# Kernel optimization log

Measured on AMD Instinct MI355X. Metric: run time of the kernel, lower is better.

The kernel has to match this reference:

```python
import jax, jax.numpy as jnp
import numpy as np

N = 100000


def gcn_conv(x, W, b, src, dst, deg_inv_sqrt, n):
    # PyG GCNConv: h = D^{-1/2} (A + I) D^{-1/2} (x W) + b
    h = x @ W  # [N, out]
    norm = deg_inv_sqrt[src] * deg_inv_sqrt[dst]  # [E+N]
    msgs = h[src] * norm[:, None]  # gathered + scaled messages
    out = jax.ops.segment_sum(msgs, dst, num_segments=n)
    return out + b


def _self_loops_and_norm(edge_index, n):
    src, dst = edge_index[0], edge_index[1]
    loop = jnp.arange(n, dtype=edge_index.dtype)
    src = jnp.concatenate([src, loop])
    dst = jnp.concatenate([dst, loop])
    deg = jax.ops.segment_sum(jnp.ones_like(dst, dtype=jnp.float32), dst, num_segments=n)
    deg_inv_sqrt = jnp.where(deg > 0, jax.lax.rsqrt(jnp.maximum(deg, 1.0)), 0.0)
    return src, dst, deg_inv_sqrt


def setup_inputs() -> dict:
    key = jax.random.key(0)
    k1, k2, k3, k4 = jax.random.split(key, 4)
    nfeat, nhid, nclass = 512, 256, 40
    E = 3200000
    x = jax.random.normal(k1, (N, nfeat), dtype=jnp.float32)
    edge_index = jax.random.randint(k2, (2, E), 0, N, dtype=jnp.int64)
    # Glorot-style init for GCNConv weights, zero bias (PyG default)
    W1 = jax.random.normal(k3, (nfeat, nhid), dtype=jnp.float32) / np.sqrt(nfeat)
    b1 = jnp.zeros((nhid,), dtype=jnp.float32)
    W2 = jax.random.normal(k4, (nhid, nclass), dtype=jnp.float32) / np.sqrt(nhid)
    b2 = jnp.zeros((nclass,), dtype=jnp.float32)
    return {"x": x, "W1": W1, "b1": b1, "W2": W2, "b2": b2, "edge_index": edge_index}


def reference(x, W1, b1, W2, b2, edge_index):
    src, dst, dis = _self_loops_and_norm(edge_index, N)
    h = gcn_conv(x, W1, b1, src, dst, dis, N)
    h = jax.nn.relu(h)
    # dropout(p=0.5) is identity in eval mode
    h = gcn_conv(h, W2, b2, src, dst, dis, N)
    return jax.nn.log_softmax(h, axis=1)
```

## Files before the change

kernel.cpp:

```cpp
#include <hip/hip_runtime.h>
#include <math.h>

#define NFEAT 512
#define NHID  256
#define NCLASS 40
#define NBUCK 782
#define BCAP  5120
#define PCHUNK 8192

typedef __attribute__((ext_vector_type(8))) short short8;
typedef __attribute__((ext_vector_type(4))) float f32x4;


__device__ __forceinline__ float bflo(unsigned u) {
    union { unsigned i; float f; } x; x.i = u << 16; return x.f;
}
__device__ __forceinline__ float bfhi(unsigned u) {
    union { unsigned i; float f; } x; x.i = u & 0xffff0000u; return x.f;
}
__device__ __forceinline__ unsigned short f2bf(float f) {
    union { float f; unsigned i; } x; x.f = f;
    unsigned r = x.i + 0x7fffu + ((x.i >> 16) & 1u);
    return (unsigned short)(r >> 16);
}
__device__ __forceinline__ float bf2f(unsigned short h) {
    union { unsigned i; float f; } x; x.i = (unsigned)h << 16; return x.f;
}
__device__ __forceinline__ unsigned pack2(float a, float b) {
    return (unsigned)f2bf(a) | ((unsigned)f2bf(b) << 16);
}


__global__ __launch_bounds__(256) void partcast_k(const float* __restrict__ W1,
                                                  unsigned short* __restrict__ WT,
                                                  const float* __restrict__ W2,
                                                  unsigned short* __restrict__ WT2,
                                                  const int* __restrict__ ei,
                                                  int* bucketCnt,
                                                  unsigned* __restrict__ binned, int E) {
    __shared__ unsigned staged[PCHUNK];
    __shared__ int hist[NBUCK];
    __shared__ int lofs[NBUCK];
    __shared__ int sbase[NBUCK];
    __shared__ int lcur[NBUCK];
    __shared__ int wsum[256];
    int bid = blockIdx.x;
    int t = threadIdx.x;
    if (bid < (NFEAT * NHID) / 256) {
        int idx = bid * 256 + t;
        int k = idx >> 8;
        int nn = idx & 255;
        WT[(size_t)nn * NFEAT + k] = f2bf(W1[idx]);
        return;
    }
    if (bid == (NFEAT * NHID) / 256) {
        for (int idx = t; idx < 96 * 256; idx += 256) {
            int j2 = idx >> 8;
            int k = idx & 255;
            int j = (j2 < 48) ? j2 : j2 - 48;
            float v = (j < NCLASS) ? W2[k * NCLASS + j] : 0.f;
            unsigned short hi = f2bf(v);
            WT2[idx] = (j2 < 48) ? hi : f2bf(v - bf2f(hi));
        }
        return;
    }
    int pb = bid - (NFEAT * NHID) / 256 - 1;
    int beg = pb * PCHUNK;
    int end = beg + PCHUNK; if (end > E) end = E;

    for (int b = t; b < NBUCK; b += 256) hist[b] = 0;
    __syncthreads();
    for (int e = beg + t; e < end; e += 256) {
        int d = ei[(size_t)E + e];
        atomicAdd(&hist[d >> 7], 1);
    }
    __syncthreads();
    int v[4];
    int s0 = 0;
#pragma unroll
    for (int r = 0; r < 4; ++r) {
        int idx = t * 4 + r;
        v[r] = (idx < NBUCK) ? hist[idx] : 0;
        s0 += v[r];
    }
    wsum[t] = s0;
    __syncthreads();
    for (int off = 1; off < 256; off <<= 1) {
        int add = (t >= off) ? wsum[t - off] : 0;
        __syncthreads();
        wsum[t] += add;
        __syncthreads();
    }
    int excl = wsum[t] - s0;
#pragma unroll
    for (int r = 0; r < 4; ++r) {
        int idx = t * 4 + r;
        if (idx < NBUCK) { lofs[idx] = excl; lcur[idx] = excl; }
        excl += v[r];
    }
    __syncthreads();
    for (int b = t; b < NBUCK; b += 256) {
        int h = hist[b];
        if (h) sbase[b] = atomicAdd(&bucketCnt[b], h);
    }
    for (int e = beg + t; e < end; e += 256) {
        int s = ei[e];
        int d = ei[(size_t)E + e];
        int b = d >> 7;
        int p = atomicAdd(&lcur[b], 1);
        staged[p] = ((unsigned)s << 7) | (unsigned)(d & 127);
    }
    __syncthreads();
    int w = t >> 6, lane = t & 63;
    for (int b = w; b < NBUCK; b += 4) {
        int h = hist[b];
        if (!h) continue;
        int lo = lofs[b];
        size_t gb = (size_t)b * BCAP + sbase[b];
        for (int l = lane; l < h; l += 64)
            binned[gb + l] = staged[lo + l];
    }
}


__global__ __launch_bounds__(1024) void bscan_k(const int* __restrict__ bucketCnt,
                                                int* __restrict__ bbase,
                                                int* __restrict__ offs, int n, int E) {
    __shared__ int sd[1024];
    int t = threadIdx.x;
    int v = (t < NBUCK) ? bucketCnt[t] : 0;
    sd[t] = v;
    __syncthreads();
    for (int off = 1; off < 1024; off <<= 1) {
        int add = (t >= off) ? sd[t - off] : 0;
        __syncthreads();
        sd[t] += add;
        __syncthreads();
    }
    if (t < NBUCK) bbase[t] = sd[t] - v;
    if (t == 0) offs[n] = E;
}


__global__ __launch_bounds__(512) void fill2_k(const unsigned* __restrict__ binned,
                                               const int* __restrict__ bucketCnt,
                                               const int* __restrict__ bbase,
                                               int* __restrict__ offs,
                                               float* __restrict__ dis,
                                               int* __restrict__ csrs, int n) {
    __shared__ int h128[128];
    __shared__ int sd[128];
    __shared__ int lcur[128];
    int b = blockIdx.x;
    int t = threadIdx.x;
    int node0 = b << 7;
    int cbt = bucketCnt[b];
    size_t base_in = (size_t)b * BCAP;
    int gbase = bbase[b];
    if (t < 128) h128[t] = 0;
    __syncthreads();
    for (int e = t; e < cbt; e += 512) {
        unsigned u = binned[base_in + e];
        atomicAdd(&h128[u & 127], 1);
    }
    __syncthreads();
    int v = (t < 128) ? h128[t] : 0;
    if (t < 128) sd[t] = v;
    __syncthreads();
    for (int off = 1; off < 128; off <<= 1) {
        int add = (t < 128 && t >= off) ? sd[t - off] : 0;
        __syncthreads();
        if (t < 128) sd[t] += add;
        __syncthreads();
    }
    if (t < 128) {
        int excl = sd[t] - v;
        int nd = node0 + t;
        if (nd < n) {
            offs[nd] = gbase + excl;
            dis[nd] = rsqrtf((float)v + 1.0f);
        }
        lcur[t] = gbase + excl;
    }
    __syncthreads();
    for (int e = t; e < cbt; e += 512) {
        unsigned u = binned[base_in + e];
        int pos = atomicAdd(&lcur[u & 127], 1);
        csrs[pos] = (int)(u >> 7);
    }
}


__global__ __launch_bounds__(512) void gemm1_k(const float* __restrict__ X,
                                               const unsigned short* __restrict__ WT,
                                               const float* __restrict__ dis,
                                               unsigned short* __restrict__ H, int M) {
    __shared__ unsigned short as[128][72];
    __shared__ unsigned short bs[256][72];
    int t = threadIdx.x;
    int lane = t & 63;
    int w = t >> 6;
    int wm = w >> 2;
    int wn = w & 3;
    int m0 = blockIdx.x * 128;
    int quad = lane >> 4;
    int r16 = lane & 15;

    f32x4 acc[4][4];
#pragma unroll
    for (int a = 0; a < 4; ++a)
#pragma unroll
        for (int b = 0; b < 4; ++b) acc[a][b] = (f32x4){0.f, 0.f, 0.f, 0.f};

    for (int k0 = 0; k0 < NFEAT; k0 += 64) {
        {
            int m = t >> 2;
            int c = (t & 3) * 16;
            int gi = m0 + m;
            float4 v0, v1, v2, v3;
            if (gi < M) {
                const float4* p = (const float4*)(X + (size_t)gi * NFEAT + k0 + c);
                v0 = p[0]; v1 = p[1]; v2 = p[2]; v3 = p[3];
            } else {
                v0 = v1 = v2 = v3 = make_float4(0.f, 0.f, 0.f, 0.f);
            }
            uint4 p0, p1;
            p0.x = pack2(v0.x, v0.y); p0.y = pack2(v0.z, v0.w);
            p0.z = pack2(v1.x, v1.y); p0.w = pack2(v1.z, v1.w);
            p1.x = pack2(v2.x, v2.y); p1.y = pack2(v2.z, v2.w);
            p1.z = pack2(v3.x, v3.y); p1.w = pack2(v3.z, v3.w);
            *(uint4*)&as[m][c] = p0;
            *(uint4*)&as[m][c + 8] = p1;
        }
        {
            int row = t >> 1;
            int ch = (t & 1) * 32;
            const uint4* p = (const uint4*)(WT + (size_t)row * NFEAT + k0 + ch);
#pragma unroll
            for (int c = 0; c < 4; ++c) {
                uint4 q = p[c];
                *(uint4*)&bs[row][ch + c * 8] = q;
            }
        }
        __syncthreads();
#pragma unroll
        for (int ks = 0; ks < 64; ks += 32) {
            short8 af[4], bfr[4];
#pragma unroll
            for (int sm = 0; sm < 4; ++sm)
                af[sm] = *(const short8*)&as[wm * 64 + sm * 16 + r16][ks + quad * 8];
#pragma unroll
            for (int sn = 0; sn < 4; ++sn)
                bfr[sn] = *(const short8*)&bs[wn * 64 + sn * 16 + r16][ks + quad * 8];
#pragma unroll
            for (int sm = 0; sm < 4; ++sm)
#pragma unroll
                for (int sn = 0; sn < 4; ++sn)
                    acc[sm][sn] = __builtin_amdgcn_mfma_f32_16x16x32_bf16(
                        af[sm], bfr[sn], acc[sm][sn], 0, 0, 0);
        }
        __syncthreads();
    }
#pragma unroll
    for (int sm = 0; sm < 4; ++sm) {
#pragma unroll
        for (int rr = 0; rr < 4; ++rr) {
            int row = m0 + wm * 64 + sm * 16 + quad * 4 + rr;
            if (row < M) {
                float dsc = dis[row];
#pragma unroll
                for (int sn = 0; sn < 4; ++sn) {
                    int col = wn * 64 + sn * 16 + r16;
                    H[(size_t)row * NHID + col] = f2bf(acc[sm][sn][rr] * dsc);
                }
            }
        }
    }
}


__global__ __launch_bounds__(256) void agg1h_k(const unsigned short* __restrict__ Hb,
                                               const int* __restrict__ offs,
                                               const int* __restrict__ csrs,
                                               const float* __restrict__ dis,
                                               const float* __restrict__ b1,
                                               unsigned short* __restrict__ outb,
                                               int n, int f0u) {
    int lane = threadIdx.x & 63;
    int i = blockIdx.x * 4 + (threadIdx.x >> 6);
    if (i >= n) return;
    const unsigned* Hv = (const unsigned*)Hb;
    int col = f0u + lane;
    float a0 = 0.f, a1 = 0.f;
    int beg = offs[i], end = offs[i + 1];
    int e = beg;
    {
        int c[16]; unsigned g[16];
        for (; e + 16 <= end; e += 16) {
#pragma unroll
            for (int u = 0; u < 16; ++u) c[u] = csrs[e + u];
#pragma unroll
            for (int u = 0; u < 16; ++u) g[u] = Hv[(size_t)c[u] * 128 + col];
#pragma unroll
            for (int u = 0; u < 16; ++u) {
                a0 += bflo(g[u]); a1 += bfhi(g[u]);
            }
        }
        if (e < end) {
#pragma unroll
            for (int u = 0; u < 16; ++u)
                c[u] = (e + u < end) ? csrs[e + u] : i;
#pragma unroll
            for (int u = 0; u < 16; ++u) g[u] = Hv[(size_t)c[u] * 128 + col];
#pragma unroll
            for (int u = 0; u < 16; ++u) {
                float sel = (e + u < end) ? 1.f : 0.f;
                a0 = fmaf(sel, bflo(g[u]), a0); a1 = fmaf(sel, bfhi(g[u]), a1);
            }
        }
    }
    unsigned v = Hv[(size_t)i * 128 + col];
    a0 += bflo(v); a1 += bfhi(v);
    float di = dis[i];
    float2 bb = ((const float2*)b1)[col];
    a0 = fmaxf(fmaf(a0, di, bb.x), 0.f);
    a1 = fmaxf(fmaf(a1, di, bb.y), 0.f);
    ((unsigned*)outb)[(size_t)i * 128 + col] = pack2(a0, a1);
}


__global__ __launch_bounds__(256) void gemm2_k(const unsigned short* __restrict__ Ab,
                                               const unsigned short* __restrict__ WT2,
                                               const float* __restrict__ dis,
                                               unsigned short* __restrict__ H2b, int M) {
    __shared__ unsigned short wt2s[96][264];
    int t = threadIdx.x;
    int lane = t & 63;
    int w = t >> 6;
    int quad = lane >> 4;
    int r16 = lane & 15;
    for (int idx = t; idx < 96 * 32; idx += 256) {
        int r = idx >> 5;
        int c = idx & 31;
        *(uint4*)&wt2s[r][c * 8] = ((const uint4*)(WT2 + (size_t)r * 256))[c];
    }
    __syncthreads();
    int row0 = blockIdx.x * 64 + w * 16;
    int gr = row0 + r16;
    f32x4 acc[3];
#pragma unroll
    for (int sn = 0; sn < 3; ++sn) acc[sn] = (f32x4){0.f, 0.f, 0.f, 0.f};
#pragma unroll
    for (int ks = 0; ks < 8; ++ks) {
        short8 af;
        if (gr < M)
            af = *(const short8*)(Ab + (size_t)gr * NHID + ks * 32 + quad * 8);
        else
            af = (short8){0, 0, 0, 0, 0, 0, 0, 0};
#pragma unroll
        for (int sn = 0; sn < 3; ++sn) {
            short8 bhi = *(const short8*)&wt2s[sn * 16 + r16][ks * 32 + quad * 8];
            short8 blo = *(const short8*)&wt2s[48 + sn * 16 + r16][ks * 32 + quad * 8];
            acc[sn] = __builtin_amdgcn_mfma_f32_16x16x32_bf16(af, bhi, acc[sn], 0, 0, 0);
            acc[sn] = __builtin_amdgcn_mfma_f32_16x16x32_bf16(af, blo, acc[sn], 0, 0, 0);
        }
    }
#pragma unroll
    for (int rr = 0; rr < 4; ++rr) {
        int row = row0 + quad * 4 + rr;
        if (row < M) {
            float dsc = dis[row];
#pragma unroll
            for (int sn = 0; sn < 3; ++sn)
                H2b[(size_t)row * 64 + sn * 16 + r16] = f2bf(acc[sn][rr] * dsc);
        }
    }
    if (lane < 32) {
        int row = row0 + r16;
        if (row < M)
            *(uint4*)&H2b[(size_t)row * 64 + 48 + (lane >> 4) * 8] =
                make_uint4(0u, 0u, 0u, 0u);
    }
}


__global__ __launch_bounds__(256) void agg2_k(const unsigned short* __restrict__ H2b,
                                              const int* __restrict__ offs,
                                              const int* __restrict__ csrs,
                                              const float* __restrict__ dis,
                                              const float* __restrict__ b2,
                                              float* __restrict__ out, int n) {
    int lane = threadIdx.x & 63;
    int i = blockIdx.x * 4 + (threadIdx.x >> 6);
    if (i >= n) return;
    const uint2* Hv = (const uint2*)H2b;
    int slot = lane >> 4;
    int r16 = lane & 15;
    float a0 = 0.f, a1 = 0.f, a2 = 0.f, a3 = 0.f;
    int beg = offs[i], end = offs[i + 1];
    int e = beg;
    {
        int c[8]; uint2 g[8];
        for (; e + 32 <= end; e += 32) {
#pragma unroll
            for (int u = 0; u < 8; ++u) c[u] = csrs[e + u * 4 + slot];
#pragma unroll
            for (int u = 0; u < 8; ++u) g[u] = Hv[(size_t)c[u] * 16 + r16];
#pragma unroll
            for (int u = 0; u < 8; ++u) {
                a0 += bflo(g[u].x); a1 += bfhi(g[u].x);
                a2 += bflo(g[u].y); a3 += bfhi(g[u].y);
            }
        }
        if (e < end) {
#pragma unroll
            for (int u = 0; u < 8; ++u) {
                int idx = e + u * 4 + slot;
                c[u] = (idx < end) ? csrs[idx] : i;
            }
#pragma unroll
            for (int u = 0; u < 8; ++u) g[u] = Hv[(size_t)c[u] * 16 + r16];
#pragma unroll
            for (int u = 0; u < 8; ++u) {
                float sel = (e + u * 4 + slot < end) ? 1.f : 0.f;
                a0 = fmaf(sel, bflo(g[u].x), a0); a1 = fmaf(sel, bfhi(g[u].x), a1);
                a2 = fmaf(sel, bflo(g[u].y), a2); a3 = fmaf(sel, bfhi(g[u].y), a3);
            }
        }
    }
    if (slot == 0) {
        uint2 v = Hv[(size_t)i * 16 + r16];
        a0 += bflo(v.x); a1 += bfhi(v.x);
        a2 += bflo(v.y); a3 += bfhi(v.y);
    }
    a0 += __shfl_xor(a0, 16, 64); a0 += __shfl_xor(a0, 32, 64);
    a1 += __shfl_xor(a1, 16, 64); a1 += __shfl_xor(a1, 32, 64);
    a2 += __shfl_xor(a2, 16, 64); a2 += __shfl_xor(a2, 32, 64);
    a3 += __shfl_xor(a3, 16, 64); a3 += __shfl_xor(a3, 32, 64);
    float di = dis[i];
    bool act = (r16 < 10);
    float4 bb = act ? ((const float4*)b2)[r16] : make_float4(0.f, 0.f, 0.f, 0.f);
    a0 = fmaf(a0, di, bb.x); a1 = fmaf(a1, di, bb.y);
    a2 = fmaf(a2, di, bb.z); a3 = fmaf(a3, di, bb.w);
    float m = act ? fmaxf(fmaxf(a0, a1), fmaxf(a2, a3)) : -INFINITY;
#pragma unroll
    for (int off = 8; off > 0; off >>= 1) m = fmaxf(m, __shfl_xor(m, off, 16));
    float s = act ? (expf(a0 - m) + expf(a1 - m) + expf(a2 - m) + expf(a3 - m)) : 0.f;
#pragma unroll
    for (int off = 8; off > 0; off >>= 1) s += __shfl_xor(s, off, 16);
    float ls = m + logf(s);
    if (lane < 10) {
        float4 o = make_float4(a0 - ls, a1 - ls, a2 - ls, a3 - ls);
        ((float4*)(out + (size_t)i * NCLASS))[lane] = o;
    }
}


extern "C" void kernel_launch(void* const* d_in, const int* in_sizes, int n_in,
                              void* d_out, int out_size, void* d_ws, size_t ws_size,
                              hipStream_t stream) {
    const float* x  = (const float*)d_in[0];
    const float* W1 = (const float*)d_in[1];
    const float* b1 = (const float*)d_in[2];
    const float* W2 = (const float*)d_in[3];
    const float* b2 = (const float*)d_in[4];
    const int*   ei = (const int*)d_in[5];

    const int N = in_sizes[0] / NFEAT;
    const int E = in_sizes[5] / 2;

    size_t off = 0;
    auto alloc = [&](size_t bytes) { size_t o = off; off += (bytes + 255) & ~(size_t)255; return o; };
    char* ws = (char*)d_ws;
    int*            offs    = (int*)           (ws + alloc((size_t)(N + 1) * 4));
    float*          dis     = (float*)         (ws + alloc((size_t)N * 4));
    int*            bcnt    = (int*)           (ws + alloc((size_t)NBUCK * 4));
    int*            bbase   = (int*)           (ws + alloc((size_t)NBUCK * 4));
    unsigned*       binned  = (unsigned*)      (ws + alloc((size_t)NBUCK * BCAP * 4));
    int*            csrs    = (int*)           (ws + alloc((size_t)E * 4));
    unsigned short* wT      = (unsigned short*)(ws + alloc((size_t)NFEAT * NHID * 2));
    unsigned short* wT2     = (unsigned short*)(ws + alloc((size_t)96 * 256 * 2));
    unsigned short* h1b     = (unsigned short*)(ws + alloc((size_t)N * NHID * 2));
    unsigned short* a1b     = (unsigned short*)(ws + alloc((size_t)N * NHID * 2));
    unsigned short* h2b     = (unsigned short*)(ws + alloc((size_t)N * 64 * 2));
    float*          out     = (float*)d_out;

    int npart = (E + PCHUNK - 1) / PCHUNK;

    hipMemsetAsync(bcnt, 0, (size_t)NBUCK * 4, stream);
    partcast_k<<<(NFEAT * NHID) / 256 + 1 + npart, 256, 0, stream>>>(W1, wT, W2, wT2, ei,
                                                                     bcnt, binned, E);
    bscan_k<<<1, 1024, 0, stream>>>(bcnt, bbase, offs, N, E);
    fill2_k<<<NBUCK, 512, 0, stream>>>(binned, bcnt, bbase, offs, dis, csrs, N);
    gemm1_k<<<(N + 127) / 128, 512, 0, stream>>>(x, wT, dis, h1b, N);
    agg1h_k<<<(N + 3) / 4, 256, 0, stream>>>(h1b, offs, csrs, dis, b1, a1b, N, 0);
    agg1h_k<<<(N + 3) / 4, 256, 0, stream>>>(h1b, offs, csrs, dis, b1, a1b, N, 64);
    gemm2_k<<<(N + 63) / 64, 256, 0, stream>>>(a1b, wT2, dis, h2b, N);
    agg2_k<<<(N + 3) / 4, 256, 0, stream>>>(h2b, offs, csrs, dis, b2, out, N);
}
```

Baseline: 715.8 us.

## Load GEMM1 operands directly from global into MFMA fragments, dropping LDS staging

The first-layer GEMM no longer stages X and W tiles through shared memory with block-wide barriers. Each wave reads its A rows (fp32, converted to bf16 in registers) and B rows straight from global memory into MFMA fragments, looping over K in 32-wide steps. This removes the LDS traffic and syncthreads, but each X row is now fetched by four waves and the per-lane loads are strided row reads, so L2/global traffic rises and coalescing worsens.

```diff
diff --git a/kernel.cpp b/kernel.cpp
--- a/kernel.cpp
+++ b/kernel.cpp
@@ -195,14 +195,12 @@
                                                const unsigned short* __restrict__ WT,
                                                const float* __restrict__ dis,
                                                unsigned short* __restrict__ H, int M) {
-    __shared__ unsigned short as[128][72];
-    __shared__ unsigned short bs[256][72];
     int t = threadIdx.x;
     int lane = t & 63;
     int w = t >> 6;
     int wm = w >> 2;
     int wn = w & 3;
-    int m0 = blockIdx.x * 128;
+    int m0 = blockIdx.x * 128 + wm * 64;
     int quad = lane >> 4;
     int r16 = lane & 15;
 
@@ -212,60 +210,49 @@
 #pragma unroll
         for (int b = 0; b < 4; ++b) acc[a][b] = (f32x4){0.f, 0.f, 0.f, 0.f};
 
-    for (int k0 = 0; k0 < NFEAT; k0 += 64) {
-        {
-            int m = t >> 2;
-            int c = (t & 3) * 16;
-            int gi = m0 + m;
-            float4 v0, v1, v2, v3;
-            if (gi < M) {
-                const float4* p = (const float4*)(X + (size_t)gi * NFEAT + k0 + c);
-                v0 = p[0]; v1 = p[1]; v2 = p[2]; v3 = p[3];
+    const unsigned short* wbase = WT + (size_t)(wn * 64 + r16) * NFEAT + quad * 8;
+    const float* abase[4];
+    bool okA[4];
+#pragma unroll
+    for (int sm = 0; sm < 4; ++sm) {
+        int row = m0 + sm * 16 + r16;
+        okA[sm] = (row < M);
+        abase[sm] = X + (size_t)(okA[sm] ? row : 0) * NFEAT + quad * 8;
+    }
+
+#pragma unroll 2
+    for (int ks = 0; ks < 16; ++ks) {
+        int ko = ks * 32;
+        short8 bfr[4];
+#pragma unroll
+        for (int sn = 0; sn < 4; ++sn)
+            bfr[sn] = *(const short8*)(wbase + (size_t)sn * 16 * NFEAT + ko);
+#pragma unroll
+        for (int sm = 0; sm < 4; ++sm) {
+            short8 af;
+            if (okA[sm]) {
+                const float4* p = (const float4*)(abase[sm] + ko);
+                float4 v0 = p[0], v1 = p[1];
+                union { uint4 u; short8 s; } cv;
+                cv.u.x = pack2(v0.x, v0.y);
+                cv.u.y = pack2(v0.z, v0.w);
+                cv.u.z = pack2(v1.x, v1.y);
+                cv.u.w = pack2(v1.z, v1.w);
+                af = cv.s;
             } else {
-                v0 = v1 = v2 = v3 = make_float4(0.f, 0.f, 0.f, 0.f);
-            }
-            uint4 p0, p1;
-            p0.x = pack2(v0.x, v0.y); p0.y = pack2(v0.z, v0.w);
-            p0.z = pack2(v1.x, v1.y); p0.w = pack2(v1.z, v1.w);
-            p1.x = pack2(v2.x, v2.y); p1.y = pack2(v2.z, v2.w);
-            p1.z = pack2(v3.x, v3.y); p1.w = pack2(v3.z, v3.w);
-            *(uint4*)&as[m][c] = p0;
-            *(uint4*)&as[m][c + 8] = p1;
-        }
-        {
-            int row = t >> 1;
-            int ch = (t & 1) * 32;
-            const uint4* p = (const uint4*)(WT + (size_t)row * NFEAT + k0 + ch);
-#pragma unroll
-            for (int c = 0; c < 4; ++c) {
-                uint4 q = p[c];
-                *(uint4*)&bs[row][ch + c * 8] = q;
-            }
-        }
-        __syncthreads();
-#pragma unroll
-        for (int ks = 0; ks < 64; ks += 32) {
-            short8 af[4], bfr[4];
-#pragma unroll
-            for (int sm = 0; sm < 4; ++sm)
-                af[sm] = *(const short8*)&as[wm * 64 + sm * 16 + r16][ks + quad * 8];
+                af = (short8){0, 0, 0, 0, 0, 0, 0, 0};
+            }
 #pragma unroll
             for (int sn = 0; sn < 4; ++sn)
-                bfr[sn] = *(const short8*)&bs[wn * 64 + sn * 16 + r16][ks + quad * 8];
-#pragma unroll
-            for (int sm = 0; sm < 4; ++sm)
-#pragma unroll
-                for (int sn = 0; sn < 4; ++sn)
-                    acc[sm][sn] = __builtin_amdgcn_mfma_f32_16x16x32_bf16(
-                        af[sm], bfr[sn], acc[sm][sn], 0, 0, 0);
-        }
-        __syncthreads();
+                acc[sm][sn] = __builtin_amdgcn_mfma_f32_16x16x32_bf16(
+                    af, bfr[sn], acc[sm][sn], 0, 0, 0);
+        }
     }
 #pragma unroll
     for (int sm = 0; sm < 4; ++sm) {
 #pragma unroll
         for (int rr = 0; rr < 4; ++rr) {
-            int row = m0 + wm * 64 + sm * 16 + quad * 4 + rr;
+            int row = m0 + sm * 16 + quad * 4 + rr;
             if (row < M) {
                 float dsc = dis[row];
 #pragma unroll
```

Measured after the change: 811.8 us. 13.4% more time.

## Pre-swizzle W1 into MFMA fragment order and load B operands directly from global

Applied to the files above, without the earlier changes.

W1 is now cast to bf16 and written in an MFMA-fragment-swizzled layout, so each lane's 8-element B fragment sits contiguously. gemm1 drops the shared-memory staging of the B tile and reads fragments straight from global/L2. This removes LDS traffic, LDS footprint and part of the barrier work per k-step, which may raise occupancy. In exchange, every block re-reads the 256 KB weight matrix from cache on each k-step with no LDS reuse across the wm wave rows.

```diff
diff --git a/kernel.cpp b/kernel.cpp
--- a/kernel.cpp
+++ b/kernel.cpp
@@ -32,7 +32,7 @@
 
 
 __global__ __launch_bounds__(256) void partcast_k(const float* __restrict__ W1,
-                                                  unsigned short* __restrict__ WT,
+                                                  unsigned short* __restrict__ WTsw,
                                                   const float* __restrict__ W2,
                                                   unsigned short* __restrict__ WT2,
                                                   const int* __restrict__ ei,
@@ -46,14 +46,20 @@
     __shared__ int wsum[256];
     int bid = blockIdx.x;
     int t = threadIdx.x;
-    if (bid < (NFEAT * NHID) / 256) {
-        int idx = bid * 256 + t;
-        int k = idx >> 8;
-        int nn = idx & 255;
-        WT[(size_t)nn * NFEAT + k] = f2bf(W1[idx]);
+    if (bid < 64) {
+        int tid = bid * 256 + t;
+        int nn = tid >> 6;
+        int k8 = tid & 63;
+        unsigned short buf[8];
+#pragma unroll
+        for (int j = 0; j < 8; ++j)
+            buf[j] = f2bf(W1[(size_t)(k8 * 8 + j) * NHID + nn]);
+        size_t dst = ((size_t)((nn >> 4) * 16 + (k8 >> 2)) * 64 +
+                      (k8 & 3) * 16 + (nn & 15)) * 8;
+        *(uint4*)(WTsw + dst) = *(const uint4*)buf;
         return;
     }
-    if (bid == (NFEAT * NHID) / 256) {
+    if (bid == 64) {
         for (int idx = t; idx < 96 * 256; idx += 256) {
             int j2 = idx >> 8;
             int k = idx & 255;
@@ -64,7 +70,7 @@
         }
         return;
     }
-    int pb = bid - (NFEAT * NHID) / 256 - 1;
+    int pb = bid - 65;
     int beg = pb * PCHUNK;
     int end = beg + PCHUNK; if (end > E) end = E;
 
@@ -192,11 +198,10 @@
 
 
 __global__ __launch_bounds__(512) void gemm1_k(const float* __restrict__ X,
-                                               const unsigned short* __restrict__ WT,
+                                               const unsigned short* __restrict__ WTsw,
                                                const float* __restrict__ dis,
                                                unsigned short* __restrict__ H, int M) {
     __shared__ unsigned short as[128][72];
-    __shared__ unsigned short bs[256][72];
     int t = threadIdx.x;
     int lane = t & 63;
     int w = t >> 6;
@@ -232,26 +237,19 @@
             *(uint4*)&as[m][c] = p0;
             *(uint4*)&as[m][c + 8] = p1;
         }
-        {
-            int row = t >> 1;
-            int ch = (t & 1) * 32;
-            const uint4* p = (const uint4*)(WT + (size_t)row * NFEAT + k0 + ch);
-#pragma unroll
-            for (int c = 0; c < 4; ++c) {
-                uint4 q = p[c];
-                *(uint4*)&bs[row][ch + c * 8] = q;
-            }
-        }
-        __syncthreads();
-#pragma unroll
-        for (int ks = 0; ks < 64; ks += 32) {
+        __syncthreads();
+        int kb0 = k0 >> 5;
+#pragma unroll
+        for (int ks = 0; ks < 2; ++ks) {
+            int kblk = kb0 + ks;
             short8 af[4], bfr[4];
 #pragma unroll
             for (int sm = 0; sm < 4; ++sm)
-                af[sm] = *(const short8*)&as[wm * 64 + sm * 16 + r16][ks + quad * 8];
+                af[sm] = *(const short8*)&as[wm * 64 + sm * 16 + r16][ks * 32 + quad * 8];
 #pragma unroll
             for (int sn = 0; sn < 4; ++sn)
-                bfr[sn] = *(const short8*)&bs[wn * 64 + sn * 16 + r16][ks + quad * 8];
+                bfr[sn] = *(const short8*)(WTsw +
+                    ((size_t)((wn * 4 + sn) * 16 + kblk) * 64 + lane) * 8);
 #pragma unroll
             for (int sm = 0; sm < 4; ++sm)
 #pragma unroll
@@ -478,7 +476,7 @@
     int*            bbase   = (int*)           (ws + alloc((size_t)NBUCK * 4));
     unsigned*       binned  = (unsigned*)      (ws + alloc((size_t)NBUCK * BCAP * 4));
     int*            csrs    = (int*)           (ws + alloc((size_t)E * 4));
-    unsigned short* wT      = (unsigned short*)(ws + alloc((size_t)NFEAT * NHID * 2));
+    unsigned short* wTsw    = (unsigned short*)(ws + alloc((size_t)NFEAT * NHID * 2));
     unsigned short* wT2     = (unsigned short*)(ws + alloc((size_t)96 * 256 * 2));
     unsigned short* h1b     = (unsigned short*)(ws + alloc((size_t)N * NHID * 2));
     unsigned short* a1b     = (unsigned short*)(ws + alloc((size_t)N * NHID * 2));
@@ -488,11 +486,10 @@
     int npart = (E + PCHUNK - 1) / PCHUNK;
 
     hipMemsetAsync(bcnt, 0, (size_t)NBUCK * 4, stream);
-    partcast_k<<<(NFEAT * NHID) / 256 + 1 + npart, 256, 0, stream>>>(W1, wT, W2, wT2, ei,
-                                                                     bcnt, binned, E);
+    partcast_k<<<65 + npart, 256, 0, stream>>>(W1, wTsw, W2, wT2, ei, bcnt, binned, E);
     bscan_k<<<1, 1024, 0, stream>>>(bcnt, bbase, offs, N, E);
     fill2_k<<<NBUCK, 512, 0, stream>>>(binned, bcnt, bbase, offs, dis, csrs, N);
-    gemm1_k<<<(N + 127) / 128, 512, 0, stream>>>(x, wT, dis, h1b, N);
+    gemm1_k<<<(N + 127) / 128, 512, 0, stream>>>(x, wTsw, dis, h1b, N);
     agg1h_k<<<(N + 3) / 4, 256, 0, stream>>>(h1b, offs, csrs, dis, b1, a1b, N, 0);
     agg1h_k<<<(N + 3) / 4, 256, 0, stream>>>(h1b, offs, csrs, dis, b1, a1b, N, 64);
     gemm2_k<<<(N + 63) / 64, 256, 0, stream>>>(a1b, wT2, dis, h2b, N);
```

New measurement: 710.5 us, median of 2. No clear change (-0.7%).
